# Kernel tuning notes

Hardware: AMD Instinct MI355X
Metric: run time of the kernel (lower is better)

Reference implementation:

```python
import jax, jax.numpy as jnp
import numpy as np

K = 20  # rec list length

def _isin(a, b, bmask=None):
    # membership of each element of a in (masked) b; a,b are small [K] int arrays
    eq = a[:, None] == b[None, :]
    if bmask is not None:
        eq = eq & bmask[None, :]
    return eq.any(axis=1)

def _compact(vals, mask):
    # stable compaction of masked elements to the front, preserving order
    n = vals.shape[0]
    order = jnp.argsort(jnp.where(mask, jnp.arange(n), n))
    return vals[order], mask.sum()

def _fuse_one(top, mid, sim, probs, key):
    # greedy set-intersection fusion of three K-length rec lists (mirrors __fuse_rec_lists)
    m_tm = _isin(top, mid)
    m_ts = _isin(top, sim)
    m_ms = _isin(mid, sim)
    # faithful to the torch code's elementwise AND of masks over different lists
    mask_common = m_tm & m_ts & m_ms
    in_common_mid = _isin(mid, top, mask_common)
    mask_tm = m_tm & ~mask_common
    mask_ts = m_ts & ~mask_common
    mask_ms = m_ms & ~in_common_mid
    top_pool_m = ~mask_common & ~mask_tm & ~mask_ts
    mid_pool_m = ~in_common_mid & ~_isin(mid, top, mask_tm) & ~mask_ms
    sim_pool_m = (~_isin(sim, top, mask_common) & ~_isin(sim, top, mask_ts)
                  & ~_isin(sim, mid, mask_ms))
    det_vals = jnp.concatenate([top, top, top, mid])          # [4K]
    det_mask = jnp.concatenate([mask_common, mask_tm, mask_ts, mask_ms])
    det, n_det = _compact(det_vals, det_mask)
    pools, counts = jax.vmap(_compact)(
        jnp.stack([top, mid, sim]),
        jnp.stack([top_pool_m, mid_pool_m, sim_pool_m]))      # [3,K], [3]
    logp = jnp.log(probs)

    def step(carry, t):
        ptr, key = carry
        key, sub = jax.random.split(key)
        avail = ptr < counts
        idx = jax.random.categorical(sub, jnp.where(avail, logp, -jnp.inf))
        sampled = pools[idx, jnp.minimum(ptr[idx], K - 1)]
        use_det = t < n_det
        val = jnp.where(use_det, det[t], sampled)
        ptr = ptr.at[idx].add(jnp.where(use_det, 0, 1))
        return (ptr, key), val

    _, out = jax.lax.scan(step, (jnp.zeros(3, jnp.int32), key), jnp.arange(K))
    return out

def setup_inputs() -> dict:
    key = jax.random.key(0)
    ks = jax.random.split(key, 9)
    B, p_dim, latent = 2048, 64, 128
    n_users, n_items = 2000, 20000
    n_top, n_mid = 2000, 5000
    rng = np.random.default_rng(0)
    perm = rng.permutation(n_items)
    return {
        "X": jax.random.normal(ks[0], (B, p_dim), jnp.float32),
        "W_sp": jax.random.normal(ks[1], (p_dim, latent), jnp.float32) * 0.1,
        "W_sd": jax.random.normal(ks[2], (latent, n_top), jnp.float32) * 0.1,
        "W_mp": jax.random.normal(ks[3], (p_dim, latent), jnp.float32) * 0.1,
        "W_md": jax.random.normal(ks[4], (latent, n_mid), jnp.float32) * 0.1,
        "W_mapper": jax.random.normal(ks[5], (p_dim, 3), jnp.float32) * 0.1,
        "user_ratings": jax.random.uniform(ks[6], (n_users, n_items), jnp.float32),
        "user_personalities": jax.random.normal(ks[7], (n_users, p_dim), jnp.float32),
        "top_map": jnp.asarray(perm[:n_top], jnp.int32),
        "mid_map": jnp.asarray(perm[n_top:n_top + n_mid], jnp.int32),
    }

def reference(X, W_sp, W_sd, W_mp, W_md, W_mapper, user_ratings,
              user_personalities, top_map, mid_map):
    B = X.shape[0]
    n_items = user_ratings.shape[1]
    # small decoder path: prior -> dec -> scatter into full item space
    top_sub = (X @ W_sp) @ W_sd                                  # [B, n_top]
    top_full = jnp.zeros((B, n_items), X.dtype).at[:, top_map].set(top_sub)
    mid_sub = (X @ W_mp) @ W_md                                  # [B, n_mid]
    mid_full = jnp.zeros((B, n_items), X.dtype).at[:, mid_map].set(mid_sub)
    # personality-similarity recommendations
    sim_scores = (X @ user_personalities.T) @ user_ratings       # [B, n_items]
    top_idx = jax.lax.top_k(top_full, K)[1].astype(jnp.int32)
    mid_idx = jax.lax.top_k(mid_full, K)[1].astype(jnp.int32)
    sim_idx = jax.lax.top_k(sim_scores, K)[1].astype(jnp.int32)
    probs = jax.nn.softmax(X @ W_mapper, axis=-1)                # [B, 3]
    keys = jax.random.split(jax.random.key(42), B)
    out = jax.vmap(_fuse_one)(top_idx, mid_idx, sim_idx, probs, keys)
    return out.astype(jnp.float32)                               # [B, K]
```

## Files before the change

kernel.cpp:

```cpp
#include <hip/hip_runtime.h>
#include <stdint.h>
#include <math.h>

#define KK 20
#define RNG_PARTITIONABLE 1


__device__ __forceinline__ void tf2x32(uint32_t k0, uint32_t k1,
                                       uint32_t c0, uint32_t c1,
                                       uint32_t& o0, uint32_t& o1) {
  const uint32_t ks2 = k0 ^ k1 ^ 0x1BD11BDAu;
  uint32_t x0 = c0 + k0, x1 = c1 + k1;
#define ROTL32(x,d) (((x) << (d)) | ((x) >> (32 - (d))))
#define R4(ra,rb,rc,rd) \
  x0 += x1; x1 = ROTL32(x1, ra); x1 ^= x0; \
  x0 += x1; x1 = ROTL32(x1, rb); x1 ^= x0; \
  x0 += x1; x1 = ROTL32(x1, rc); x1 ^= x0; \
  x0 += x1; x1 = ROTL32(x1, rd); x1 ^= x0;
  R4(13,15,26,6);  x0 += k1;  x1 += ks2 + 1u;
  R4(17,29,16,24); x0 += ks2; x1 += k0 + 2u;
  R4(13,15,26,6);  x0 += k0;  x1 += k1 + 3u;
  R4(17,29,16,24); x0 += k1;  x1 += ks2 + 4u;
  R4(13,15,26,6);  x0 += ks2; x1 += k0 + 5u;
  o0 = x0; o1 = x1;
#undef R4
#undef ROTL32
}

__device__ __forceinline__ float u01_from_bits(uint32_t b) {
  float f = __uint_as_float((b >> 9) | 0x3f800000u) - 1.0f;
  return (f == 0.0f) ? 1.17549435e-38f : f;
}

#define GK 16

__device__ __forceinline__ void gemm_nn_body(
    const float* __restrict__ A, int lda,
    const float* __restrict__ Bg, int ldb,
    float* __restrict__ C, int ldc,
    int M, int N, int K, int kc,
    float (*As)[68], float (*Bs)[132]) {
  const int tid = threadIdx.x;
  const int row0 = blockIdx.y * 64;
  const int col0 = blockIdx.x * 128;
  const int tr = tid >> 4, tc = tid & 15;
  const int kc_eff = (kc > 0) ? kc : K;

  const int a_ar = tid >> 2, a_ac = (tid & 3) << 2;
  int b_br[2], b_bc[2];
#pragma unroll
  for (int i = 0; i < 2; ++i) { int s = tid + i * 256; b_br[i] = s >> 5; b_bc[i] = (s & 31) << 2; }

  float4 pa, pb[2];
  auto load_regs = [&](int k0) {
    {
      int gr = row0 + a_ar, gc = k0 + a_ac;
      float4 v = make_float4(0.f, 0.f, 0.f, 0.f);
      if (gr < M) {
        if (gc + 3 < K) v = *(const float4*)(A + (size_t)gr * lda + gc);
        else {
          float t0 = (gc     < K) ? A[(size_t)gr * lda + gc]     : 0.f;
          float t1 = (gc + 1 < K) ? A[(size_t)gr * lda + gc + 1] : 0.f;
          float t2 = (gc + 2 < K) ? A[(size_t)gr * lda + gc + 2] : 0.f;
          float t3 = (gc + 3 < K) ? A[(size_t)gr * lda + gc + 3] : 0.f;
          v = make_float4(t0, t1, t2, t3);
        }
      }
      pa = v;
    }
#pragma unroll
    for (int i = 0; i < 2; ++i) {
      int gk = k0 + b_br[i], gc = col0 + b_bc[i];
      float4 v = make_float4(0.f, 0.f, 0.f, 0.f);
      if (gk < K) {
        if (gc + 3 < N) v = *(const float4*)(Bg + (size_t)gk * ldb + gc);
        else {
          float t0 = (gc     < N) ? Bg[(size_t)gk * ldb + gc]     : 0.f;
          float t1 = (gc + 1 < N) ? Bg[(size_t)gk * ldb + gc + 1] : 0.f;
          float t2 = (gc + 2 < N) ? Bg[(size_t)gk * ldb + gc + 2] : 0.f;
          float t3 = (gc + 3 < N) ? Bg[(size_t)gk * ldb + gc + 3] : 0.f;
          v = make_float4(t0, t1, t2, t3);
        }
      }
      pb[i] = v;
    }
  };
  auto store_lds = [&](int buf) {
    float (*Ab)[68] = As + buf * GK;
    float (*Bb)[132] = Bs + buf * GK;
    Ab[a_ac + 0][a_ar] = pa.x; Ab[a_ac + 1][a_ar] = pa.y;
    Ab[a_ac + 2][a_ar] = pa.z; Ab[a_ac + 3][a_ar] = pa.w;
#pragma unroll
    for (int i = 0; i < 2; ++i) *(float4*)&Bb[b_br[i]][b_bc[i]] = pb[i];
  };

  float accM[4][8];
#pragma unroll
  for (int i = 0; i < 4; ++i)
#pragma unroll
    for (int j = 0; j < 8; ++j) accM[i][j] = 0.f;

  for (int c0 = 0; c0 < K; c0 += kc_eff) {
    const int kend = (c0 + kc_eff < K) ? (c0 + kc_eff) : K;
    const int ntile = (kend - c0 + GK - 1) / GK;
    float acc[4][8];
#pragma unroll
    for (int i = 0; i < 4; ++i)
#pragma unroll
      for (int j = 0; j < 8; ++j) acc[i][j] = 0.f;

    load_regs(c0);
    store_lds(0);
    __syncthreads();
    int cur = 0;
    for (int t = 0; t < ntile; ++t) {
      const int k0 = c0 + t * GK;
      const bool has_next = (t + 1 < ntile);
      if (has_next) load_regs(k0 + GK);
      float (*Ab)[68] = As + cur * GK;
      float (*Bb)[132] = Bs + cur * GK;
      const int klim = (kend - k0 < GK) ? (kend - k0) : GK;
      for (int kk = 0; kk < klim; ++kk) {
        float4 av = *(const float4*)&Ab[kk][tr << 2];
        float4 b0 = *(const float4*)&Bb[kk][tc << 2];
        float4 b1 = *(const float4*)&Bb[kk][64 + (tc << 2)];
        float a[4] = {av.x, av.y, av.z, av.w};
        float b[8] = {b0.x, b0.y, b0.z, b0.w, b1.x, b1.y, b1.z, b1.w};
#pragma unroll
        for (int i = 0; i < 4; ++i)
#pragma unroll
          for (int j = 0; j < 8; ++j)
            acc[i][j] = __fadd_rn(acc[i][j], __fmul_rn(a[i], b[j]));
      }
      if (has_next) {
        store_lds(1 - cur);
        __syncthreads();
        cur ^= 1;
      }
    }
    __syncthreads();
#pragma unroll
    for (int i = 0; i < 4; ++i)
#pragma unroll
      for (int j = 0; j < 8; ++j) accM[i][j] = __fadd_rn(accM[i][j], acc[i][j]);
  }
#pragma unroll
  for (int i = 0; i < 4; ++i) {
    int gr = row0 + (tr << 2) + i;
    if (gr >= M) continue;
#pragma unroll
    for (int j = 0; j < 8; ++j) {
      int gc = col0 + ((j < 4) ? (tc << 2) + j : 64 + (tc << 2) + (j - 4));
      if (gc < N) C[(size_t)gr * ldc + gc] = accM[i][j];
    }
  }
}

__global__ __launch_bounds__(256) void gemm_nn_k(
    const float* __restrict__ A, int lda,
    const float* __restrict__ Bg, int ldb,
    float* __restrict__ C, int ldc,
    int M, int N, int K, int kc) {
  __shared__ __align__(16) float As[2 * GK][68];
  __shared__ __align__(16) float Bs[2 * GK][132];
  gemm_nn_body(A, lda, Bg, ldb, C, ldc, M, N, K, kc, As, Bs);
}

__global__ __launch_bounds__(256) void gemm_prior_k(
    const float* __restrict__ X,
    const float* __restrict__ Wsp, const float* __restrict__ Wmp,
    float* __restrict__ Ht, float* __restrict__ Hm,
    int B, int P, int L) {
  __shared__ __align__(16) float As[2 * GK][68];
  __shared__ __align__(16) float Bs[2 * GK][132];
  if (blockIdx.z == 0)
    gemm_nn_body(X, P, Wsp, L, Ht, L, B, L, P, 0, As, Bs);
  else
    gemm_nn_body(X, P, Wmp, L, Hm, L, B, L, P, 0, As, Bs);
}

__global__ __launch_bounds__(256) void gemm_nt_k(
    const float* __restrict__ A, int lda,
    const float* __restrict__ Bg, int ldb,
    float* __restrict__ C, int ldc,
    int M, int N, int K) {
  __shared__ __align__(16) float As[16][128 + 4];
  __shared__ __align__(16) float Bs[16][128 + 4];
  const int tid = threadIdx.x;
  const int row0 = blockIdx.y * 128;
  const int col0 = blockIdx.x * 128;
  const int tr = tid >> 4, tc = tid & 15;
  float acc[8][8];
#pragma unroll
  for (int i = 0; i < 8; ++i)
#pragma unroll
    for (int j = 0; j < 8; ++j) acc[i][j] = 0.f;

  for (int k0 = 0; k0 < K; k0 += 16) {
#pragma unroll
    for (int i = 0; i < 2; ++i) {
      int s = tid + i * 256;
      int ar = s >> 2, ac = (s & 3) << 2;
      int gr = row0 + ar, gc = k0 + ac;
      float4 v = make_float4(0.f, 0.f, 0.f, 0.f);
      if (gr < M) {
        if (gc + 3 < K) v = *(const float4*)(A + (size_t)gr * lda + gc);
        else {
          float t0 = (gc     < K) ? A[(size_t)gr * lda + gc]     : 0.f;
          float t1 = (gc + 1 < K) ? A[(size_t)gr * lda + gc + 1] : 0.f;
          float t2 = (gc + 2 < K) ? A[(size_t)gr * lda + gc + 2] : 0.f;
          float t3 = (gc + 3 < K) ? A[(size_t)gr * lda + gc + 3] : 0.f;
          v = make_float4(t0, t1, t2, t3);
        }
      }
      As[ac + 0][ar] = v.x; As[ac + 1][ar] = v.y;
      As[ac + 2][ar] = v.z; As[ac + 3][ar] = v.w;
    }
#pragma unroll
    for (int i = 0; i < 2; ++i) {
      int s = tid + i * 256;
      int nr = s >> 2, kcc = (s & 3) << 2;
      int gn = col0 + nr, gk = k0 + kcc;
      float4 v = make_float4(0.f, 0.f, 0.f, 0.f);
      if (gn < N) {
        if (gk + 3 < K) v = *(const float4*)(Bg + (size_t)gn * ldb + gk);
        else {
          float t0 = (gk     < K) ? Bg[(size_t)gn * ldb + gk]     : 0.f;
          float t1 = (gk + 1 < K) ? Bg[(size_t)gn * ldb + gk + 1] : 0.f;
          float t2 = (gk + 2 < K) ? Bg[(size_t)gn * ldb + gk + 2] : 0.f;
          float t3 = (gk + 3 < K) ? Bg[(size_t)gn * ldb + gk + 3] : 0.f;
          v = make_float4(t0, t1, t2, t3);
        }
      }
      Bs[kcc + 0][nr] = v.x; Bs[kcc + 1][nr] = v.y;
      Bs[kcc + 2][nr] = v.z; Bs[kcc + 3][nr] = v.w;
    }
    __syncthreads();
#pragma unroll
    for (int kk = 0; kk < 16; ++kk) {
      float4 a0 = *(const float4*)&As[kk][tr * 8];
      float4 a1 = *(const float4*)&As[kk][tr * 8 + 4];
      float4 b0 = *(const float4*)&Bs[kk][tc * 8];
      float4 b1 = *(const float4*)&Bs[kk][tc * 8 + 4];
      float a[8] = {a0.x, a0.y, a0.z, a0.w, a1.x, a1.y, a1.z, a1.w};
      float b[8] = {b0.x, b0.y, b0.z, b0.w, b1.x, b1.y, b1.z, b1.w};
#pragma unroll
      for (int i = 0; i < 8; ++i)
#pragma unroll
        for (int j = 0; j < 8; ++j)
          acc[i][j] = __fadd_rn(acc[i][j], __fmul_rn(a[i], b[j]));
    }
    __syncthreads();
  }
#pragma unroll
  for (int i = 0; i < 8; ++i) {
    int gr = row0 + tr * 8 + i;
    if (gr >= M) continue;
#pragma unroll
    for (int j = 0; j < 8; ++j) {
      int gc = col0 + tc * 8 + j;
      if (gc < N) C[(size_t)gr * ldc + gc] = acc[i][j];
    }
  }
}

__device__ __forceinline__ void topk20_row(
    const float* __restrict__ row, int ncols, int col_off,
    const int* __restrict__ map,
    float* __restrict__ SV, int* __restrict__ SI, int merge,
    float (*shv)[KK], int (*shi)[KK], float* ov, int* oi) {
  const int t = threadIdx.x;
  float lv[KK]; int li[KK];
#pragma unroll
  for (int i = 0; i < KK; ++i) { lv[i] = -INFINITY; li[i] = 0x7fffffff; }
  for (int c = t; c < ncols; c += 256) {
    float v = row[c];
    if (v > lv[KK - 1]) {
      float cv = v; int ci = c;
#pragma unroll
      for (int i = 0; i < KK; ++i) {
        bool sw = cv > lv[i];
        float tv = lv[i]; int ti = li[i];
        lv[i] = sw ? cv : tv; li[i] = sw ? ci : ti;
        cv = sw ? tv : cv;    ci = sw ? ti : ci;
      }
    }
  }
#pragma unroll
  for (int i = 0; i < KK; ++i) { shv[t][i] = lv[i]; shi[t][i] = li[i]; }
  __syncthreads();
  if (t < 64) {
    int hp0 = 0, hp1 = 0, hp2 = 0, hp3 = 0;
    for (int round = 0; round < KK; ++round) {
      int base = t * 4;
      float v0 = (hp0 < KK) ? shv[base + 0][hp0] : -INFINITY;
      int   i0 = (hp0 < KK) ? shi[base + 0][hp0] : 0x7fffffff;
      float v1 = (hp1 < KK) ? shv[base + 1][hp1] : -INFINITY;
      int   i1 = (hp1 < KK) ? shi[base + 1][hp1] : 0x7fffffff;
      float v2 = (hp2 < KK) ? shv[base + 2][hp2] : -INFINITY;
      int   i2 = (hp2 < KK) ? shi[base + 2][hp2] : 0x7fffffff;
      float v3 = (hp3 < KK) ? shv[base + 3][hp3] : -INFINITY;
      int   i3 = (hp3 < KK) ? shi[base + 3][hp3] : 0x7fffffff;
      float bv = v0; int bi = i0; int bq = 0;
      if (v1 > bv || (v1 == bv && i1 < bi)) { bv = v1; bi = i1; bq = 1; }
      if (v2 > bv || (v2 == bv && i2 < bi)) { bv = v2; bi = i2; bq = 2; }
      if (v3 > bv || (v3 == bv && i3 < bi)) { bv = v3; bi = i3; bq = 3; }
      float cv = bv; int ci = bi; int cl = t; int cq = bq;
#pragma unroll
      for (int s2 = 1; s2 < 64; s2 <<= 1) {
        float vx = __shfl_xor(cv, s2);
        int   ix = __shfl_xor(ci, s2);
        int   lx = __shfl_xor(cl, s2);
        int   qx = __shfl_xor(cq, s2);
        if (vx > cv || (vx == cv && ix < ci)) { cv = vx; ci = ix; cl = lx; cq = qx; }
      }
      if (t == 0) { ov[round] = cv; oi[round] = ci; }
      if (cl == t) { hp0 += (cq == 0); hp1 += (cq == 1); hp2 += (cq == 2); hp3 += (cq == 3); }
    }
    if (t == 0) {
      if (!merge) {
        for (int i = 0; i < KK; ++i) {
          SV[i] = ov[i];
          SI[i] = map ? map[oi[i]] : (oi[i] + col_off);
        }
      } else {
        float mv[KK]; int mi[KK];
        int a = 0, b = 0;
        for (int i = 0; i < KK; ++i) {
          float va = SV[a]; int ia = SI[a];
          float vb = ov[b]; int ib = oi[b] + col_off;
          bool ta = (va > vb) || (va == vb && ia < ib);
          if (ta) { mv[i] = va; mi[i] = ia; ++a; }
          else    { mv[i] = vb; mi[i] = ib; ++b; }
        }
        for (int i = 0; i < KK; ++i) { SV[i] = mv[i]; SI[i] = mi[i]; }
      }
    }
  }
}

__global__ __launch_bounds__(256) void topk20_k(
    const float* __restrict__ mat, int ld, int ncols, int col_off,
    const int* __restrict__ map,
    float* __restrict__ sval, int* __restrict__ sidx, int merge) {
  __shared__ float shv[256][KK];
  __shared__ int   shi[256][KK];
  __shared__ float ov[KK];
  __shared__ int   oi[KK];
  const int r = blockIdx.x;
  topk20_row(mat + (size_t)r * ld, ncols, col_off, map,
             sval + (size_t)r * KK, sidx + (size_t)r * KK, merge, shv, shi, ov, oi);
}

__global__ __launch_bounds__(256) void topk20_dual_k(
    const float* __restrict__ m0, int nc0, const int* __restrict__ map0,
    float* __restrict__ sv0, int* __restrict__ si0,
    const float* __restrict__ m1, int nc1, const int* __restrict__ map1,
    float* __restrict__ sv1, int* __restrict__ si1) {
  __shared__ float shv[256][KK];
  __shared__ int   shi[256][KK];
  __shared__ float ov[KK];
  __shared__ int   oi[KK];
  const int r = blockIdx.x;
  if (blockIdx.y == 0)
    topk20_row(m0 + (size_t)r * nc0, nc0, 0, map0,
               sv0 + (size_t)r * KK, si0 + (size_t)r * KK, 0, shv, shi, ov, oi);
  else
    topk20_row(m1 + (size_t)r * nc1, nc1, 0, map1,
               sv1 + (size_t)r * KK, si1 + (size_t)r * KK, 0, shv, shi, ov, oi);
}

__global__ __launch_bounds__(256) void fuse_k(
    const float* __restrict__ X, const float* __restrict__ Wmap,
    const int* __restrict__ siT, const int* __restrict__ siM,
    const int* __restrict__ siS, float* __restrict__ out, int B) {
  int r = blockIdx.x * blockDim.x + threadIdx.x;
  if (r >= B) return;
  int top[KK], mid[KK], sim[KK];
  for (int i = 0; i < KK; ++i) {
    top[i] = siT[(size_t)r * KK + i];
    mid[i] = siM[(size_t)r * KK + i];
    sim[i] = siS[(size_t)r * KK + i];
  }
  float z0 = 0.f, z1 = 0.f, z2 = 0.f;
  for (int k = 0; k < 64; ++k) {
    float x = X[(size_t)r * 64 + k];
    z0 = __fadd_rn(z0, __fmul_rn(x, Wmap[k * 3 + 0]));
    z1 = __fadd_rn(z1, __fmul_rn(x, Wmap[k * 3 + 1]));
    z2 = __fadd_rn(z2, __fmul_rn(x, Wmap[k * 3 + 2]));
  }
  float zm = fmaxf(z0, fmaxf(z1, z2));
  float e0 = expf(z0 - zm), e1 = expf(z1 - zm), e2 = expf(z2 - zm);
  float s = __fadd_rn(__fadd_rn(e0, e1), e2);
  float logp[3] = { logf(__fdiv_rn(e0, s)), logf(__fdiv_rn(e1, s)), logf(__fdiv_rn(e2, s)) };
  bool m_tm[KK], m_ts[KK], m_ms[KK], maskC[KK], inCmid[KK], mTM[KK], mTS[KK], mMS[KK];
  for (int i = 0; i < KK; ++i) {
    bool a = false, b = false, c = false;
    for (int j = 0; j < KK; ++j) {
      a |= (top[i] == mid[j]);
      b |= (top[i] == sim[j]);
      c |= (mid[i] == sim[j]);
    }
    m_tm[i] = a; m_ts[i] = b; m_ms[i] = c;
  }
  for (int i = 0; i < KK; ++i) maskC[i] = m_tm[i] && m_ts[i] && m_ms[i];
  for (int i = 0; i < KK; ++i) {
    bool v = false;
    for (int j = 0; j < KK; ++j) v |= (mid[i] == top[j]) && maskC[j];
    inCmid[i] = v;
  }
  for (int i = 0; i < KK; ++i) {
    mTM[i] = m_tm[i] && !maskC[i];
    mTS[i] = m_ts[i] && !maskC[i];
    mMS[i] = m_ms[i] && !inCmid[i];
  }
  bool poolT[KK], poolM[KK], poolS[KK];
  for (int i = 0; i < KK; ++i) poolT[i] = !maskC[i] && !mTM[i] && !mTS[i];
  for (int i = 0; i < KK; ++i) {
    bool v = false;
    for (int j = 0; j < KK; ++j) v |= (mid[i] == top[j]) && mTM[j];
    poolM[i] = !inCmid[i] && !v && !mMS[i];
  }
  for (int i = 0; i < KK; ++i) {
    bool v1 = false, v2 = false, v3 = false;
    for (int j = 0; j < KK; ++j) {
      v1 |= (sim[i] == top[j]) && maskC[j];
      v2 |= (sim[i] == top[j]) && mTS[j];
      v3 |= (sim[i] == mid[j]) && mMS[j];
    }
    poolS[i] = !v1 && !v2 && !v3;
  }
  int det[KK]; int ndet = 0;
  for (int i = 0; i < KK; ++i) if (maskC[i]) { if (ndet < KK) det[ndet] = top[i]; ndet++; }
  for (int i = 0; i < KK; ++i) if (mTM[i])  { if (ndet < KK) det[ndet] = top[i]; ndet++; }
  for (int i = 0; i < KK; ++i) if (mTS[i])  { if (ndet < KK) det[ndet] = top[i]; ndet++; }
  for (int i = 0; i < KK; ++i) if (mMS[i])  { if (ndet < KK) det[ndet] = mid[i]; ndet++; }
  int pool[3][KK]; int cnt[3];
  {
    int c = 0;
    for (int i = 0; i < KK; ++i) if (poolT[i]) pool[0][c++] = top[i];
    cnt[0] = c;
    for (int i = 0; i < KK; ++i) if (!poolT[i]) pool[0][c++] = top[i];
  }
  {
    int c = 0;
    for (int i = 0; i < KK; ++i) if (poolM[i]) pool[1][c++] = mid[i];
    cnt[1] = c;
    for (int i = 0; i < KK; ++i) if (!poolM[i]) pool[1][c++] = mid[i];
  }
  {
    int c = 0;
    for (int i = 0; i < KK; ++i) if (poolS[i]) pool[2][c++] = sim[i];
    cnt[2] = c;
    for (int i = 0; i < KK; ++i) if (!poolS[i]) pool[2][c++] = sim[i];
  }
  uint32_t k0, k1;
#if RNG_PARTITIONABLE
  { uint32_t a, b; tf2x32(0u, 42u, 0u, (uint32_t)r, a, b); k0 = a; k1 = b; }
#else
  {
    if (r < 1024) {
      uint32_t x0, x1, y0, y1;
      tf2x32(0u, 42u, (uint32_t)(2 * r),     (uint32_t)(2048 + 2 * r),     x0, x1);
      tf2x32(0u, 42u, (uint32_t)(2 * r + 1), (uint32_t)(2048 + 2 * r + 1), y0, y1);
      k0 = x0; k1 = y0;
    } else {
      int j = 2 * r - 2048;
      uint32_t x0, x1, y0, y1;
      tf2x32(0u, 42u, (uint32_t)j,       (uint32_t)(2048 + j),     x0, x1);
      tf2x32(0u, 42u, (uint32_t)(j + 1), (uint32_t)(2048 + j + 1), y0, y1);
      k0 = x1; k1 = y1;
    }
  }
#endif
  int ptr0 = 0, ptr1 = 0, ptr2 = 0;
  for (int t = 0; t < KK; ++t) {
    uint32_t nk0, nk1, sb0, sb1;
#if RNG_PARTITIONABLE
    tf2x32(k0, k1, 0u, 0u, nk0, nk1);
    tf2x32(k0, k1, 0u, 1u, sb0, sb1);
#else
    { uint32_t p0x, p0y, p1x, p1y;
      tf2x32(k0, k1, 0u, 2u, p0x, p0y);
      tf2x32(k0, k1, 1u, 3u, p1x, p1y);
      nk0 = p0x; nk1 = p1x; sb0 = p0y; sb1 = p1y; }
#endif
    k0 = nk0; k1 = nk1;
    float g[3];
#if RNG_PARTITIONABLE
    for (int i = 0; i < 3; ++i) {
      uint32_t a, b; tf2x32(sb0, sb1, 0u, (uint32_t)i, a, b);
      float u = u01_from_bits(a ^ b);
      g[i] = -logf(-logf(u));
    }
#else
    { uint32_t q0x, q0y, q1x, q1y;
      tf2x32(sb0, sb1, 0u, 2u, q0x, q0y);
      tf2x32(sb0, sb1, 1u, 0u, q1x, q1y);
      uint32_t bits[3] = { q0x, q1x, q0y };
      for (int i = 0; i < 3; ++i) {
        float u = u01_from_bits(bits[i]);
        g[i] = -logf(-logf(u));
      }
    }
#endif
    float s0 = (ptr0 < cnt[0]) ? g[0] + logp[0] : -INFINITY;
    float s1 = (ptr1 < cnt[1]) ? g[1] + logp[1] : -INFINITY;
    float s2 = (ptr2 < cnt[2]) ? g[2] + logp[2] : -INFINITY;
    int idx = 0; float best = s0;
    if (s1 > best) { best = s1; idx = 1; }
    if (s2 > best) { best = s2; idx = 2; }
    int p = (idx == 0) ? ptr0 : ((idx == 1) ? ptr1 : ptr2);
    int sampled = pool[idx][p < (KK - 1) ? p : (KK - 1)];
    int val = (t < ndet) ? det[t] : sampled;
    out[(size_t)r * KK + t] = (float)val;
    if (t >= ndet) { if (idx == 0) ++ptr0; else if (idx == 1) ++ptr1; else ++ptr2; }
  }
}

extern "C" void kernel_launch(void* const* d_in, const int* in_sizes, int n_in,
                              void* d_out, int out_size, void* d_ws, size_t ws_size,
                              hipStream_t stream) {
  const float* X    = (const float*)d_in[0];
  const float* Wsp  = (const float*)d_in[1];
  const float* Wsd  = (const float*)d_in[2];
  const float* Wmp  = (const float*)d_in[3];
  const float* Wmd  = (const float*)d_in[4];
  const float* Wmap = (const float*)d_in[5];
  const float* R    = (const float*)d_in[6];
  const float* U    = (const float*)d_in[7];
  const int* top_map = (const int*)d_in[8];
  const int* mid_map = (const int*)d_in[9];
  float* out = (float*)d_out;

  const int B = 2048, P_DIM = 64, LAT = 128;
  const int N_TOP = 2000, N_MID = 5000, N_USERS = 2000, N_ITEMS = 20000;
  const int CHUNK = 5000, N_CHUNKS = 4;
  const int KC_EIGEN = 320;
  (void)in_sizes; (void)n_in; (void)out_size;

  char* ws = (char*)d_ws;
  size_t off = 0;
  auto alloc = [&](size_t bytes) -> void* {
    off = (off + 255) & ~(size_t)255;
    void* p = ws + off; off += bytes; return p;
  };

  const size_t BIG_NEED = (size_t)B * (2 * LAT + N_USERS + N_TOP + N_MID + N_ITEMS + 6 * KK) * 4
                          + 16 * 256;
  const bool big = (ws_size >= BIG_NEED);

  dim3 blk(256);
  if (big) {
    float* Ht  = (float*)alloc((size_t)B * LAT * 4);
    float* Hm  = (float*)alloc((size_t)B * LAT * 4);
    float* Pm  = (float*)alloc((size_t)B * N_USERS * 4);
    float* CHt = (float*)alloc((size_t)B * N_TOP * 4);
    float* CHm = (float*)alloc((size_t)B * N_MID * 4);
    float* CHs = (float*)alloc((size_t)B * N_ITEMS * 4);
    float* svT = (float*)alloc((size_t)B * KK * 4);
    int*   siT = (int*)  alloc((size_t)B * KK * 4);
    float* svM = (float*)alloc((size_t)B * KK * 4);
    int*   siM = (int*)  alloc((size_t)B * KK * 4);
    float* svS = (float*)alloc((size_t)B * KK * 4);
    int*   siS = (int*)  alloc((size_t)B * KK * 4);

    gemm_prior_k<<<dim3(1, 32, 2), blk, 0, stream>>>(X, Wsp, Wmp, Ht, Hm, B, P_DIM, LAT);
    gemm_nn_k<<<dim3(16, 32), blk, 0, stream>>>(Ht, LAT, Wsd, N_TOP, CHt, N_TOP, B, N_TOP, LAT, 0);
    gemm_nn_k<<<dim3(40, 32), blk, 0, stream>>>(Hm, LAT, Wmd, N_MID, CHm, N_MID, B, N_MID, LAT, 0);
    topk20_dual_k<<<dim3(B, 2), blk, 0, stream>>>(CHt, N_TOP, top_map, svT, siT,
                                                  CHm, N_MID, mid_map, svM, siM);
    gemm_nt_k<<<dim3(16, 16), blk, 0, stream>>>(X, P_DIM, U, P_DIM, Pm, N_USERS, B, N_USERS, P_DIM);
    for (int c = 0; c < N_CHUNKS; ++c) {
      gemm_nn_k<<<dim3(40, 32), blk, 0, stream>>>(Pm, N_USERS, R + (size_t)c * CHUNK, N_ITEMS,
                                                  CHs + (size_t)c * CHUNK, N_ITEMS,
                                                  B, CHUNK, N_USERS, KC_EIGEN);
    }
    topk20_k<<<dim3(B), blk, 0, stream>>>(CHs, N_ITEMS, N_ITEMS, 0, nullptr, svS, siS, 0);
    fuse_k<<<dim3(B / 256), blk, 0, stream>>>(X, Wmap, siT, siM, siS, out, B);
  } else {
    float* H   = (float*)alloc((size_t)B * LAT * 4);
    float* Pm  = (float*)alloc((size_t)B * N_USERS * 4);
    float* CH  = (float*)alloc((size_t)B * CHUNK * 4);
    float* svT = (float*)alloc((size_t)B * KK * 4);
    int*   siT = (int*)  alloc((size_t)B * KK * 4);
    float* svM = (float*)alloc((size_t)B * KK * 4);
    int*   siM = (int*)  alloc((size_t)B * KK * 4);
    float* svS = (float*)alloc((size_t)B * KK * 4);
    int*   siS = (int*)  alloc((size_t)B * KK * 4);

    gemm_nn_k<<<dim3(1, 32), blk, 0, stream>>>(X, P_DIM, Wsp, LAT, H, LAT, B, LAT, P_DIM, 0);
    gemm_nn_k<<<dim3(16, 32), blk, 0, stream>>>(H, LAT, Wsd, N_TOP, CH, N_TOP, B, N_TOP, LAT, 0);
    topk20_k<<<dim3(B), blk, 0, stream>>>(CH, N_TOP, N_TOP, 0, top_map, svT, siT, 0);
    gemm_nn_k<<<dim3(1, 32), blk, 0, stream>>>(X, P_DIM, Wmp, LAT, H, LAT, B, LAT, P_DIM, 0);
    gemm_nn_k<<<dim3(40, 32), blk, 0, stream>>>(H, LAT, Wmd, N_MID, CH, N_MID, B, N_MID, LAT, 0);
    topk20_k<<<dim3(B), blk, 0, stream>>>(CH, N_MID, N_MID, 0, mid_map, svM, siM, 0);
    gemm_nt_k<<<dim3(16, 16), blk, 0, stream>>>(X, P_DIM, U, P_DIM, Pm, N_USERS, B, N_USERS, P_DIM);
    for (int c = 0; c < N_CHUNKS; ++c) {
      gemm_nn_k<<<dim3(40, 32), blk, 0, stream>>>(Pm, N_USERS, R + (size_t)c * CHUNK, N_ITEMS,
                                                  CH, CHUNK, B, CHUNK, N_USERS, KC_EIGEN);
      topk20_k<<<dim3(B), blk, 0, stream>>>(CH, CHUNK, CHUNK, c * CHUNK, nullptr, svS, siS, c ? 1 : 0);
    }
    fuse_k<<<dim3(B / 256), blk, 0, stream>>>(X, Wmap, siT, siM, siS, out, B);
  }
}
```

Measured before the change: 3.494 ms.

## Drop GEMM LDS double-buffering and use nontemporal stores for large score outputs

```diff
diff --git a/kernel.cpp b/kernel.cpp
--- a/kernel.cpp
+++ b/kernel.cpp
@@ -34,6 +34,7 @@
 
 #define GK 16
 
+template <bool NT>
 __device__ __forceinline__ void gemm_nn_body(
     const float* __restrict__ A, int lda,
     const float* __restrict__ Bg, int ldb,
@@ -45,55 +46,6 @@
   const int col0 = blockIdx.x * 128;
   const int tr = tid >> 4, tc = tid & 15;
   const int kc_eff = (kc > 0) ? kc : K;
-
-  const int a_ar = tid >> 2, a_ac = (tid & 3) << 2;
-  int b_br[2], b_bc[2];
-#pragma unroll
-  for (int i = 0; i < 2; ++i) { int s = tid + i * 256; b_br[i] = s >> 5; b_bc[i] = (s & 31) << 2; }
-
-  float4 pa, pb[2];
-  auto load_regs = [&](int k0) {
-    {
-      int gr = row0 + a_ar, gc = k0 + a_ac;
-      float4 v = make_float4(0.f, 0.f, 0.f, 0.f);
-      if (gr < M) {
-        if (gc + 3 < K) v = *(const float4*)(A + (size_t)gr * lda + gc);
-        else {
-          float t0 = (gc     < K) ? A[(size_t)gr * lda + gc]     : 0.f;
-          float t1 = (gc + 1 < K) ? A[(size_t)gr * lda + gc + 1] : 0.f;
-          float t2 = (gc + 2 < K) ? A[(size_t)gr * lda + gc + 2] : 0.f;
-          float t3 = (gc + 3 < K) ? A[(size_t)gr * lda + gc + 3] : 0.f;
-          v = make_float4(t0, t1, t2, t3);
-        }
-      }
-      pa = v;
-    }
-#pragma unroll
-    for (int i = 0; i < 2; ++i) {
-      int gk = k0 + b_br[i], gc = col0 + b_bc[i];
-      float4 v = make_float4(0.f, 0.f, 0.f, 0.f);
-      if (gk < K) {
-        if (gc + 3 < N) v = *(const float4*)(Bg + (size_t)gk * ldb + gc);
-        else {
-          float t0 = (gc     < N) ? Bg[(size_t)gk * ldb + gc]     : 0.f;
-          float t1 = (gc + 1 < N) ? Bg[(size_t)gk * ldb + gc + 1] : 0.f;
-          float t2 = (gc + 2 < N) ? Bg[(size_t)gk * ldb + gc + 2] : 0.f;
-          float t3 = (gc + 3 < N) ? Bg[(size_t)gk * ldb + gc + 3] : 0.f;
-          v = make_float4(t0, t1, t2, t3);
-        }
-      }
-      pb[i] = v;
-    }
-  };
-  auto store_lds = [&](int buf) {
-    float (*Ab)[68] = As + buf * GK;
-    float (*Bb)[132] = Bs + buf * GK;
-    Ab[a_ac + 0][a_ar] = pa.x; Ab[a_ac + 1][a_ar] = pa.y;
-    Ab[a_ac + 2][a_ar] = pa.z; Ab[a_ac + 3][a_ar] = pa.w;
-#pragma unroll
-    for (int i = 0; i < 2; ++i) *(float4*)&Bb[b_br[i]][b_bc[i]] = pb[i];
-  };
-
   float accM[4][8];
 #pragma unroll
   for (int i = 0; i < 4; ++i)
@@ -102,28 +54,54 @@
 
   for (int c0 = 0; c0 < K; c0 += kc_eff) {
     const int kend = (c0 + kc_eff < K) ? (c0 + kc_eff) : K;
-    const int ntile = (kend - c0 + GK - 1) / GK;
     float acc[4][8];
 #pragma unroll
     for (int i = 0; i < 4; ++i)
 #pragma unroll
       for (int j = 0; j < 8; ++j) acc[i][j] = 0.f;
 
-    load_regs(c0);
-    store_lds(0);
-    __syncthreads();
-    int cur = 0;
-    for (int t = 0; t < ntile; ++t) {
-      const int k0 = c0 + t * GK;
-      const bool has_next = (t + 1 < ntile);
-      if (has_next) load_regs(k0 + GK);
-      float (*Ab)[68] = As + cur * GK;
-      float (*Bb)[132] = Bs + cur * GK;
+    for (int k0 = c0; k0 < kend; k0 += GK) {
+      {
+        int ar = tid >> 2, ac = (tid & 3) << 2;
+        int gr = row0 + ar, gc = k0 + ac;
+        float4 v = make_float4(0.f, 0.f, 0.f, 0.f);
+        if (gr < M) {
+          if (gc + 3 < K) v = *(const float4*)(A + (size_t)gr * lda + gc);
+          else {
+            float t0 = (gc     < K) ? A[(size_t)gr * lda + gc]     : 0.f;
+            float t1 = (gc + 1 < K) ? A[(size_t)gr * lda + gc + 1] : 0.f;
+            float t2 = (gc + 2 < K) ? A[(size_t)gr * lda + gc + 2] : 0.f;
+            float t3 = (gc + 3 < K) ? A[(size_t)gr * lda + gc + 3] : 0.f;
+            v = make_float4(t0, t1, t2, t3);
+          }
+        }
+        As[ac + 0][ar] = v.x; As[ac + 1][ar] = v.y;
+        As[ac + 2][ar] = v.z; As[ac + 3][ar] = v.w;
+      }
+#pragma unroll
+      for (int i = 0; i < 2; ++i) {
+        int s = tid + i * 256;
+        int br = s >> 5, bc = (s & 31) << 2;
+        int gk = k0 + br, gc = col0 + bc;
+        float4 v = make_float4(0.f, 0.f, 0.f, 0.f);
+        if (gk < K) {
+          if (gc + 3 < N) v = *(const float4*)(Bg + (size_t)gk * ldb + gc);
+          else {
+            float t0 = (gc     < N) ? Bg[(size_t)gk * ldb + gc]     : 0.f;
+            float t1 = (gc + 1 < N) ? Bg[(size_t)gk * ldb + gc + 1] : 0.f;
+            float t2 = (gc + 2 < N) ? Bg[(size_t)gk * ldb + gc + 2] : 0.f;
+            float t3 = (gc + 3 < N) ? Bg[(size_t)gk * ldb + gc + 3] : 0.f;
+            v = make_float4(t0, t1, t2, t3);
+          }
+        }
+        *(float4*)&Bs[br][bc] = v;
+      }
+      __syncthreads();
       const int klim = (kend - k0 < GK) ? (kend - k0) : GK;
       for (int kk = 0; kk < klim; ++kk) {
-        float4 av = *(const float4*)&Ab[kk][tr << 2];
-        float4 b0 = *(const float4*)&Bb[kk][tc << 2];
-        float4 b1 = *(const float4*)&Bb[kk][64 + (tc << 2)];
+        float4 av = *(const float4*)&As[kk][tr << 2];
+        float4 b0 = *(const float4*)&Bs[kk][tc << 2];
+        float4 b1 = *(const float4*)&Bs[kk][64 + (tc << 2)];
         float a[4] = {av.x, av.y, av.z, av.w};
         float b[8] = {b0.x, b0.y, b0.z, b0.w, b1.x, b1.y, b1.z, b1.w};
 #pragma unroll
@@ -132,13 +110,8 @@
           for (int j = 0; j < 8; ++j)
             acc[i][j] = __fadd_rn(acc[i][j], __fmul_rn(a[i], b[j]));
       }
-      if (has_next) {
-        store_lds(1 - cur);
-        __syncthreads();
-        cur ^= 1;
-      }
-    }
-    __syncthreads();
+      __syncthreads();
+    }
 #pragma unroll
     for (int i = 0; i < 4; ++i)
 #pragma unroll
@@ -151,7 +124,10 @@
 #pragma unroll
     for (int j = 0; j < 8; ++j) {
       int gc = col0 + ((j < 4) ? (tc << 2) + j : 64 + (tc << 2) + (j - 4));
-      if (gc < N) C[(size_t)gr * ldc + gc] = accM[i][j];
+      if (gc < N) {
+        if (NT) __builtin_nontemporal_store(accM[i][j], C + (size_t)gr * ldc + gc);
+        else    C[(size_t)gr * ldc + gc] = accM[i][j];
+      }
     }
   }
 }
@@ -161,9 +137,19 @@
     const float* __restrict__ Bg, int ldb,
     float* __restrict__ C, int ldc,
     int M, int N, int K, int kc) {
-  __shared__ __align__(16) float As[2 * GK][68];
-  __shared__ __align__(16) float Bs[2 * GK][132];
-  gemm_nn_body(A, lda, Bg, ldb, C, ldc, M, N, K, kc, As, Bs);
+  __shared__ __align__(16) float As[GK][68];
+  __shared__ __align__(16) float Bs[GK][132];
+  gemm_nn_body<false>(A, lda, Bg, ldb, C, ldc, M, N, K, kc, As, Bs);
+}
+
+__global__ __launch_bounds__(256) void gemm_nn_nt_k(
+    const float* __restrict__ A, int lda,
+    const float* __restrict__ Bg, int ldb,
+    float* __restrict__ C, int ldc,
+    int M, int N, int K, int kc) {
+  __shared__ __align__(16) float As[GK][68];
+  __shared__ __align__(16) float Bs[GK][132];
+  gemm_nn_body<true>(A, lda, Bg, ldb, C, ldc, M, N, K, kc, As, Bs);
 }
 
 __global__ __launch_bounds__(256) void gemm_prior_k(
@@ -171,12 +157,12 @@
     const float* __restrict__ Wsp, const float* __restrict__ Wmp,
     float* __restrict__ Ht, float* __restrict__ Hm,
     int B, int P, int L) {
-  __shared__ __align__(16) float As[2 * GK][68];
-  __shared__ __align__(16) float Bs[2 * GK][132];
+  __shared__ __align__(16) float As[GK][68];
+  __shared__ __align__(16) float Bs[GK][132];
   if (blockIdx.z == 0)
-    gemm_nn_body(X, P, Wsp, L, Ht, L, B, L, P, 0, As, Bs);
+    gemm_nn_body<false>(X, P, Wsp, L, Ht, L, B, L, P, 0, As, Bs);
   else
-    gemm_nn_body(X, P, Wmp, L, Hm, L, B, L, P, 0, As, Bs);
+    gemm_nn_body<false>(X, P, Wmp, L, Hm, L, B, L, P, 0, As, Bs);
 }
 
 __global__ __launch_bounds__(256) void gemm_nt_k(
@@ -566,15 +552,15 @@
     int*   siS = (int*)  alloc((size_t)B * KK * 4);
 
     gemm_prior_k<<<dim3(1, 32, 2), blk, 0, stream>>>(X, Wsp, Wmp, Ht, Hm, B, P_DIM, LAT);
-    gemm_nn_k<<<dim3(16, 32), blk, 0, stream>>>(Ht, LAT, Wsd, N_TOP, CHt, N_TOP, B, N_TOP, LAT, 0);
-    gemm_nn_k<<<dim3(40, 32), blk, 0, stream>>>(Hm, LAT, Wmd, N_MID, CHm, N_MID, B, N_MID, LAT, 0);
+    gemm_nn_nt_k<<<dim3(16, 32), blk, 0, stream>>>(Ht, LAT, Wsd, N_TOP, CHt, N_TOP, B, N_TOP, LAT, 0);
+    gemm_nn_nt_k<<<dim3(40, 32), blk, 0, stream>>>(Hm, LAT, Wmd, N_MID, CHm, N_MID, B, N_MID, LAT, 0);
     topk20_dual_k<<<dim3(B, 2), blk, 0, stream>>>(CHt, N_TOP, top_map, svT, siT,
                                                   CHm, N_MID, mid_map, svM, siM);
     gemm_nt_k<<<dim3(16, 16), blk, 0, stream>>>(X, P_DIM, U, P_DIM, Pm, N_USERS, B, N_USERS, P_DIM);
     for (int c = 0; c < N_CHUNKS; ++c) {
-      gemm_nn_k<<<dim3(40, 32), blk, 0, stream>>>(Pm, N_USERS, R + (size_t)c * CHUNK, N_ITEMS,
-                                                  CHs + (size_t)c * CHUNK, N_ITEMS,
-                                                  B, CHUNK, N_USERS, KC_EIGEN);
+      gemm_nn_nt_k<<<dim3(40, 32), blk, 0, stream>>>(Pm, N_USERS, R + (size_t)c * CHUNK, N_ITEMS,
+                                                     CHs + (size_t)c * CHUNK, N_ITEMS,
+                                                     B, CHUNK, N_USERS, KC_EIGEN);
     }
     topk20_k<<<dim3(B), blk, 0, stream>>>(CHs, N_ITEMS, N_ITEMS, 0, nullptr, svS, siS, 0);
     fuse_k<<<dim3(B / 256), blk, 0, stream>>>(X, Wmap, siT, siM, siS, out, B);
```

After: 3.952 ms. +13.1%, slower.
